# Kernel tuning notes

Hardware: AMD Instinct MI355X
Metric: run time of the kernel (lower is better)

## Reference

```python
import jax, jax.numpy as jnp
import numpy as np

N = 16384
IN_DIM = 11
D = 64
L = 4
K = 16 + 1  # self.k + 1 (n >= k+1)
EPS = 1e-5


def _bn(x, g, b):
    # BatchNorm1d in training mode: biased batch stats over the edge/node axis
    m = jnp.mean(x, axis=0)
    v = jnp.var(x, axis=0)
    return g * (x - m) * jax.lax.rsqrt(v + EPS) + b


def _mlp(x, W1, b1, g1, be1, W2, b2, g2, be2):
    x = jax.nn.relu(_bn(x @ W1 + b1, g1, be1))
    x = jax.nn.relu(_bn(x @ W2 + b2, g2, be2))
    return x


def _knn_edges(h):
    # torch.cdist + topk(-d, K); row 0 of idx.T is the (self) nearest node
    hs = jax.lax.stop_gradient(h)  # only indices are used downstream
    sq = jnp.sum(hs * hs, axis=-1)
    d2 = sq[:, None] + sq[None, :] - 2.0 * (hs @ hs.T)  # (n, n)
    d = jnp.sqrt(jnp.maximum(d2, 0.0))
    _, idx = jax.lax.top_k(-d, K)  # (n, K)
    frm = jnp.tile(idx[:, 0], K - 1)            # from_nodes = row0 repeated
    to = idx[:, 1:].T.reshape(-1)               # to_nodes = rows 1..K-1 flattened
    return frm, to


def setup_inputs() -> dict:
    key = jax.random.key(0)
    ks = jax.random.split(key, 8)
    s = 0.05
    inp = {
        "pos": jax.random.normal(ks[0], (N, IN_DIM), jnp.float32),
        "lin_in_W": jax.random.normal(ks[1], (IN_DIM, D), jnp.float32) * s,
        "lin_in_b": jnp.zeros((D,), jnp.float32),
        "pred_W": jax.random.normal(ks[2], (D, 1), jnp.float32) * s,
        "pred_b": jnp.zeros((1,), jnp.float32),
    }
    i = 3
    for pre in ("msg", "upd"):
        inp[f"{pre}_W1"] = jax.random.normal(ks[i], (L, 2 * D, D), jnp.float32) * s
        inp[f"{pre}_b1"] = jnp.zeros((L, D), jnp.float32)
        inp[f"{pre}_g1"] = jnp.ones((L, D), jnp.float32)
        inp[f"{pre}_be1"] = jnp.zeros((L, D), jnp.float32)
        inp[f"{pre}_W2"] = jax.random.normal(ks[i + 1], (L, D, D), jnp.float32) * s
        inp[f"{pre}_b2"] = jnp.zeros((L, D), jnp.float32)
        inp[f"{pre}_g2"] = jnp.ones((L, D), jnp.float32)
        inp[f"{pre}_be2"] = jnp.zeros((L, D), jnp.float32)
        i += 2
    return inp


def reference(pos, lin_in_W, lin_in_b, pred_W, pred_b,
              msg_W1, msg_b1, msg_g1, msg_be1, msg_W2, msg_b2, msg_g2, msg_be2,
              upd_W1, upd_b1, upd_g1, upd_be1, upd_W2, upd_b2, upd_g2, upd_be2):
    h = pos @ lin_in_W + lin_in_b  # (n, d)
    for l in range(L):
        frm, to = _knn_edges(h)
        # PyG source_to_target: h_j = h[edge_index[0]] (source), h_i = h[edge_index[1]] (dest)
        h_i = h[to]
        h_j = h[frm]
        msg = _mlp(jnp.concatenate([h_i, h_j], axis=-1),
                   msg_W1[l], msg_b1[l], msg_g1[l], msg_be1[l],
                   msg_W2[l], msg_b2[l], msg_g2[l], msg_be2[l])  # (e, d)
        agg = jax.ops.segment_sum(msg, to, num_segments=N)  # scatter-add at dest
        upd = _mlp(jnp.concatenate([h, agg], axis=-1),
                   upd_W1[l], upd_b1[l], upd_g1[l], upd_be1[l],
                   upd_W2[l], upd_b2[l], upd_g2[l], upd_be2[l])
        h = h + upd  # residual
    h_graph = jnp.mean(h, axis=0, keepdims=True)  # global_mean_pool, single graph
    out = h_graph @ pred_W + pred_b
    return out.reshape(-1)
```

## Files before the change

### kernel.cpp

```cpp
#include <hip/hip_runtime.h>

#define NN 16384
#define KP1 17
#define EE (NN*16)
#define CAP 448

typedef short bf16x8 __attribute__((ext_vector_type(8)));
typedef float f32x16 __attribute__((ext_vector_type(16)));

__device__ __forceinline__ ushort f2bf(float f) {
  unsigned u = __float_as_uint(f);
  unsigned r = (u + 0x7fffu + ((u >> 16) & 1u)) >> 16;
  return (ushort)r;
}
__device__ __forceinline__ float bf2f(ushort s) { return __uint_as_float(((unsigned)s) << 16); }

__global__ __launch_bounds__(256) void k_lin_in(const float* __restrict__ pos,
    const float* __restrict__ W, const float* __restrict__ b, float* __restrict__ h) {
  const int t = blockIdx.x*256 + threadIdx.x;
  const int n = t >> 6, c = t & 63;
  float acc = b[c];
  #pragma unroll
  for (int k = 0; k < 11; ++k) acc = fmaf(pos[n*11+k], W[k*64+c], acc);
  h[t] = acc;
}

__global__ __launch_bounds__(256) void k_prep_all(const float* __restrict__ h, float* __restrict__ sq,
    ushort* __restrict__ pk, ushort* __restrict__ hbh, ushort* __restrict__ hbl) {
  const int row = blockIdx.x*256 + threadIdx.x;
  const int tile = row >> 5, rl = row & 31;
  const float4* rp = (const float4*)(h + (size_t)row*64);
  float s = 0.f;
  #pragma unroll
  for (int q = 0; q < 16; ++q) {
    const float4 x = rp[q];
    s += x.x*x.x + x.y*x.y + x.z*x.z + x.w*x.w;
    ushort4 hi, lo;
    hi.x = f2bf(x.x); lo.x = f2bf(x.x - bf2f(hi.x));
    hi.y = f2bf(x.y); lo.y = f2bf(x.y - bf2f(hi.y));
    hi.z = f2bf(x.z); lo.z = f2bf(x.z - bf2f(hi.z));
    hi.w = f2bf(x.w); lo.w = f2bf(x.w - bf2f(hi.w));
    *(ushort4*)(hbh + (size_t)row*64 + q*4) = hi;
    *(ushort4*)(hbl + (size_t)row*64 + q*4) = lo;
    const int ks = q >> 2, sub = (q >> 1) & 1, e = (q & 1)*4;
    const int lane = rl + 32*sub;
    ushort* base = pk + (size_t)tile*4096 + ks*1024 + (size_t)lane*8 + e;
    *(ushort4*)(base)       = hi;
    *(ushort4*)(base + 512) = lo;
  }
  sq[row] = s;
}

__global__ __launch_bounds__(256) void k_wprep(const float* __restrict__ W1all,
    const float* __restrict__ W2all, ushort* __restrict__ wp1, ushort* __restrict__ wp2) {
  const int t = blockIdx.x*256 + threadIdx.x;
  if (t < 4096) {
    const int lane = t & 63, ks = (t>>6)&7, mt = (t>>9)&1, l = t>>10;
    const int m = mt*32 + (lane&31);
    const int k0 = ks*16 + (lane>>5)*8;
    const float* w = W1all + l*8192;
    ushort* dst = wp1 + ((((size_t)l*2 + mt)*8 + ks)*2)*512 + (size_t)lane*8;
    #pragma unroll
    for (int e = 0; e < 8; ++e) {
      const float v = w[(k0+e)*64 + m];
      const ushort hi = f2bf(v);
      dst[e] = hi; dst[512+e] = f2bf(v - bf2f(hi));
    }
  } else if (t < 6144) {
    const int t2 = t - 4096;
    const int lane = t2 & 63, ks = (t2>>6)&3, mt = (t2>>8)&1, l = t2>>9;
    const int m = mt*32 + (lane&31);
    const int k0 = ks*16 + (lane>>5)*8;
    const float* w = W2all + l*4096;
    ushort* dst = wp2 + ((((size_t)l*2 + mt)*4 + ks)*2)*512 + (size_t)lane*8;
    #pragma unroll
    for (int e = 0; e < 8; ++e) {
      const float v = w[(k0+e)*64 + m];
      const ushort hi = f2bf(v);
      dst[e] = hi; dst[512+e] = f2bf(v - bf2f(hi));
    }
  }
}

struct F8 { bf16x8 h0,h1,h2,h3,l0,l1,l2,l3; };

__device__ __forceinline__ void ldf(const ushort* __restrict__ pk, int tile, int lane, F8& f) {
  const ushort* tp = pk + (size_t)tile*4096 + (size_t)lane*8;
  f.h0 = *(const bf16x8*)(tp);
  f.l0 = *(const bf16x8*)(tp + 512);
  f.h1 = *(const bf16x8*)(tp + 1024);
  f.l1 = *(const bf16x8*)(tp + 1536);
  f.h2 = *(const bf16x8*)(tp + 2048);
  f.l2 = *(const bf16x8*)(tp + 2560);
  f.h3 = *(const bf16x8*)(tp + 3072);
  f.l3 = *(const bf16x8*)(tp + 3584);
}

#define MF(A,B,C) __builtin_amdgcn_mfma_f32_32x32x16_bf16(A,B,C,0,0,0)

__device__ __forceinline__ void tile_keys(const F8& f, const bf16x8 (&bqh)[4], const bf16x8 (&bql)[4],
    const float* __restrict__ sq, const int tile, const int lhi, float (&key)[16]) {
  f32x16 acc;
  #pragma unroll
  for (int i = 0; i < 16; ++i) acc[i] = 0.f;
  acc = MF(f.h0, bqh[0], acc); acc = MF(f.h0, bql[0], acc); acc = MF(f.l0, bqh[0], acc);
  acc = MF(f.h1, bqh[1], acc); acc = MF(f.h1, bql[1], acc); acc = MF(f.l1, bqh[1], acc);
  acc = MF(f.h2, bqh[2], acc); acc = MF(f.h2, bql[2], acc); acc = MF(f.l2, bqh[2], acc);
  acc = MF(f.h3, bqh[3], acc); acc = MF(f.h3, bql[3], acc); acc = MF(f.l3, bqh[3], acc);
  const int c0 = tile*32;
  #pragma unroll
  for (int g = 0; g < 4; ++g) {
    const float4 v = *(const float4*)(sq + c0 + g*8 + 4*lhi);
    key[g*4+0] = fmaf(-2.f, acc[g*4+0], v.x);
    key[g*4+1] = fmaf(-2.f, acc[g*4+1], v.y);
    key[g*4+2] = fmaf(-2.f, acc[g*4+2], v.z);
    key[g*4+3] = fmaf(-2.f, acc[g*4+3], v.w);
  }
}

#define HIST1(K) { _Pragma("unroll") for (int r = 0; r < 16; ++r) { \
    unsigned x = __float_as_uint(K[r]); x = (x & 0x80000000u) ? ~x : (x | 0x80000000u); \
    atomicAdd(&hist[x >> 24][qcol], 1u); } }
#define HIST2(K) { _Pragma("unroll") for (int r = 0; r < 16; ++r) { \
    unsigned x = __float_as_uint(K[r]); x = (x & 0x80000000u) ? ~x : (x | 0x80000000u); \
    if ((x >> 24) == b1) atomicAdd(&hist[(x >> 16) & 255u][qcol], 1u); } }
#define COLLECT(K, TILE) { _Pragma("unroll") for (int r = 0; r < 16; ++r) { \
    if (K[r] <= bfq) { \
      unsigned x = __float_as_uint(K[r]); x = (x & 0x80000000u) ? ~x : (x | 0x80000000u); \
      const unsigned slot = atomicAdd(&ccnt[qcol], 1u); \
      if (slot < CAP) { \
        const int cidx = (TILE)*32 + (r & 3) + 8*(r >> 2) + 4*lhi; \
        coll[(size_t)q*CAP + slot] = ((unsigned long long)x << 32) | (unsigned)cidx; } } } }

__global__ __launch_bounds__(512) void k_knn(const ushort* __restrict__ pk,
    const float* __restrict__ sq, unsigned long long* __restrict__ coll,
    unsigned* __restrict__ gcnt) {
  __shared__ unsigned hist[256][32];
  __shared__ unsigned bin1s[32], below1s[32];
  __shared__ float boundf[32];
  __shared__ unsigned ccnt[32];
  const int tid = threadIdx.x;
  const int wave = tid >> 6, lane = tid & 63;
  const int qcol = lane & 31, lhi = lane >> 5;
  const int qt = blockIdx.x;
  const int q = qt*32 + qcol;

  for (int i = tid; i < 256*32; i += 512) ((unsigned*)hist)[i] = 0u;
  if (tid < 32) ccnt[tid] = 0u;

  bf16x8 bqh[4], bql[4];
  {
    const ushort* tp = pk + (size_t)qt*4096 + (size_t)lane*8;
    #pragma unroll
    for (int ks = 0; ks < 4; ++ks) {
      bqh[ks] = *(const bf16x8*)(tp + ks*1024);
      bql[ks] = *(const bf16x8*)(tp + ks*1024 + 512);
    }
  }
  __syncthreads();

  {
    F8 fa, fb;
    ldf(pk, wave*8, lane, fa);
    #pragma unroll 1
    for (int s = 0; s < 8; s += 2) {
      ldf(pk, wave*8 + s + 1, lane, fb);
      float k0[16]; tile_keys(fa, bqh, bql, sq, wave*8 + s, lhi, k0);
      HIST1(k0)
      if (s + 2 < 8) ldf(pk, wave*8 + s + 2, lane, fa);
      float k1[16]; tile_keys(fb, bqh, bql, sq, wave*8 + s + 1, lhi, k1);
      HIST1(k1)
    }
  }
  __syncthreads();
  if (tid < 32) {
    unsigned c = 0, b = 0, bl_ = 0, fnd = 0;
    #pragma unroll 1
    for (int i = 0; i < 256; ++i) {
      const unsigned nc = c + hist[i][tid];
      if (!fnd && nc >= KP1) { b = (unsigned)i; bl_ = c; fnd = 1; }
      c = nc;
    }
    bin1s[tid] = b; below1s[tid] = bl_;
  }
  __syncthreads();
  for (int i = tid; i < 256*32; i += 512) ((unsigned*)hist)[i] = 0u;
  __syncthreads();
  const unsigned b1 = bin1s[qcol];

  {
    F8 fa, fb;
    ldf(pk, wave*8, lane, fa);
    #pragma unroll 1
    for (int s = 0; s < 8; s += 2) {
      ldf(pk, wave*8 + s + 1, lane, fb);
      float k0[16]; tile_keys(fa, bqh, bql, sq, wave*8 + s, lhi, k0);
      HIST2(k0)
      if (s + 2 < 8) ldf(pk, wave*8 + s + 2, lane, fa);
      float k1[16]; tile_keys(fb, bqh, bql, sq, wave*8 + s + 1, lhi, k1);
      HIST2(k1)
    }
  }
  __syncthreads();
  if (tid < 32) {
    unsigned c = below1s[tid], b = 255u, fnd = 0;
    #pragma unroll 1
    for (int i = 0; i < 256; ++i) {
      c += hist[i][tid];
      if (!fnd && c >= KP1) { b = (unsigned)i; fnd = 1; }
    }
    const unsigned bu = (bin1s[tid] << 24) | (b << 16) | 0xFFFFu;
    boundf[tid] = __uint_as_float((bu & 0x80000000u) ? (bu & 0x7fffffffu) : ~bu);
  }
  __syncthreads();
  const float bfq = boundf[qcol];

  {
    F8 fa, fb;
    ldf(pk, wave*64, lane, fa);
    #pragma unroll 1
    for (int s = 0; s < 64; s += 2) {
      ldf(pk, wave*64 + s + 1, lane, fb);
      float k0[16]; tile_keys(fa, bqh, bql, sq, wave*64 + s, lhi, k0);
      COLLECT(k0, wave*64 + s)
      if (s + 2 < 64) ldf(pk, wave*64 + s + 2, lane, fa);
      float k1[16]; tile_keys(fb, bqh, bql, sq, wave*64 + s + 1, lhi, k1);
      COLLECT(k1, wave*64 + s + 1)
    }
  }
  __syncthreads();
  if (tid < 32) gcnt[qt*32 + tid] = min(ccnt[tid], (unsigned)CAP);
}

__global__ __launch_bounds__(256) void k_select(const unsigned long long* __restrict__ coll,
    const unsigned* __restrict__ gcnt, int* __restrict__ idxout) {
  const int gw = (blockIdx.x*256 + threadIdx.x) >> 6;
  const int lane = threadIdx.x & 63;
  const int m = min((int)gcnt[gw], CAP);
  const unsigned long long* cp = coll + (size_t)gw*CAP;
  unsigned long long a0,a1,a2,a3,a4,a5,a6;
  a0 = (lane       < m) ? cp[lane      ] : ~0ULL;
  a1 = (lane +  64 < m) ? cp[lane +  64] : ~0ULL;
  a2 = (lane + 128 < m) ? cp[lane + 128] : ~0ULL;
  a3 = (lane + 192 < m) ? cp[lane + 192] : ~0ULL;
  a4 = (lane + 256 < m) ? cp[lane + 256] : ~0ULL;
  a5 = (lane + 320 < m) ? cp[lane + 320] : ~0ULL;
  a6 = (lane + 384 < m) ? cp[lane + 384] : ~0ULL;
  #define CS(X,Y) { if (Y < X) { const unsigned long long t_ = X; X = Y; Y = t_; } }
  CS(a0,a1) CS(a2,a3) CS(a4,a5)
  CS(a1,a2) CS(a3,a4) CS(a5,a6)
  CS(a0,a1) CS(a2,a3) CS(a4,a5)
  CS(a1,a2) CS(a3,a4) CS(a5,a6)
  CS(a0,a1) CS(a2,a3) CS(a4,a5)
  CS(a1,a2) CS(a3,a4) CS(a5,a6)
  CS(a0,a1) CS(a2,a3) CS(a4,a5)
  #undef CS
  #pragma unroll
  for (int p = 0; p < KP1; ++p) {
    unsigned long long w = a0;
    #pragma unroll
    for (int d = 1; d < 64; d <<= 1) {
      const unsigned long long o = __shfl_xor(w, d);
      w = o < w ? o : w;
    }
    if (lane == 0) idxout[gw*KP1 + p] = (int)(unsigned)(w & 0xffffffffULL);
    if (a0 == w) { a0=a1; a1=a2; a2=a3; a3=a4; a4=a5; a5=a6; a6=~0ULL; }
  }
}

__global__ __launch_bounds__(256) void k_cnt(const int* __restrict__ idx, unsigned* __restrict__ cnt) {
  const int e = blockIdx.x*256 + threadIdx.x;
  const int i = e & (NN-1), k = e >> 14;
  atomicAdd(&cnt[idx[i*KP1 + k + 1]], 1u);
}

__global__ __launch_bounds__(256) void k_scan(const unsigned* __restrict__ cnt,
    unsigned* __restrict__ offs, unsigned* __restrict__ pos) {
  __shared__ unsigned ps[256];
  const int t = threadIdx.x;
  unsigned s = 0;
  #pragma unroll 4
  for (int j = 0; j < 64; ++j) s += cnt[t*64 + j];
  ps[t] = s;
  __syncthreads();
  for (int d = 1; d < 256; d <<= 1) {
    const unsigned v = (t >= d) ? ps[t-d] : 0u;
    __syncthreads();
    ps[t] += v;
    __syncthreads();
  }
  unsigned run = ps[t] - s;
  #pragma unroll 4
  for (int j = 0; j < 64; ++j) {
    const unsigned c = cnt[t*64 + j];
    offs[t*64 + j] = run; pos[t*64 + j] = run;
    run += c;
  }
}

__global__ __launch_bounds__(256) void k_scatter(const int* __restrict__ idx,
    unsigned* __restrict__ pos, unsigned* __restrict__ sortedE) {
  const int e = blockIdx.x*256 + threadIdx.x;
  const int i = e & (NN-1), k = e >> 14;
  const int to = idx[i*KP1 + k + 1];
  sortedE[atomicAdd(&pos[to], 1u)] = (unsigned)e;
}

__global__ __launch_bounds__(256) void k_agg(const ushort* __restrict__ y2,
    const unsigned* __restrict__ offs, const unsigned* __restrict__ cnt,
    const unsigned* __restrict__ sortedE,
    const float* __restrict__ s, const float* __restrict__ s2,
    const float* __restrict__ gam, const float* __restrict__ bet, float* __restrict__ agg) {
  __shared__ float scs[64], shs[64];
  const int tid = threadIdx.x;
  if (tid < 64) {
    const float m = s[tid] * (1.f/(float)EE);
    const float v = fmaxf(s2[tid]*(1.f/(float)EE) - m*m, 0.f);
    const float scv = gam[tid]*rsqrtf(v + 1e-5f);
    scs[tid] = scv; shs[tid] = bet[tid] - m*scv;
  }
  __syncthreads();
  const int t = blockIdx.x*256 + tid;
  const int n = t >> 4, c4 = t & 15;
  const unsigned o = offs[n], m = cnt[n];
  const float sc0 = scs[c4*4+0], sc1 = scs[c4*4+1], sc2 = scs[c4*4+2], sc3 = scs[c4*4+3];
  const float sh0 = shs[c4*4+0], sh1 = shs[c4*4+1], sh2 = shs[c4*4+2], sh3 = shs[c4*4+3];
  float a0=0.f, a1=0.f, a2=0.f, a3=0.f;
  for (unsigned j = 0; j < m; ++j) {
    const unsigned e = sortedE[o + j];
    const ushort4 v = *(const ushort4*)(y2 + (size_t)e*64 + c4*4);
    a0 += fmaxf(fmaf(bf2f(v.x), sc0, sh0), 0.f);
    a1 += fmaxf(fmaf(bf2f(v.y), sc1, sh1), 0.f);
    a2 += fmaxf(fmaf(bf2f(v.z), sc2, sh2), 0.f);
    a3 += fmaxf(fmaf(bf2f(v.w), sc3, sh3), 0.f);
  }
  *(float4*)(agg + (size_t)n*64 + c4*4) = make_float4(a0, a1, a2, a3);
}

__global__ __launch_bounds__(256) void k_eA(const ushort* __restrict__ hbh,
    const ushort* __restrict__ hbl, const int* __restrict__ idx,
    const ushort* __restrict__ wp1, const float* __restrict__ b1, ushort* __restrict__ y1) {
  __shared__ ushort wlds[16384];
  __shared__ float b1s[64];
  __shared__ ushort ytr[4][32][40];
  const int tid = threadIdx.x, wave = tid >> 6, lane = tid & 63;
  const int n = lane & 31, lhi = lane >> 5;
  for (int i = tid*8; i < 16384; i += 2048) *(uint4*)(wlds+i) = *(const uint4*)(wp1+i);
  if (tid < 64) b1s[tid] = b1[tid];
  __syncthreads();

  const int tile = blockIdx.x*4 + wave;
  const int e = tile*32 + n;
  const int i_ = e & (NN-1), kk = e >> 14;
  const int to = idx[i_*KP1 + kk + 1];
  const int fr = idx[i_*KP1];

  bf16x8 bh[8], bl[8];
  #pragma unroll
  for (int ks = 0; ks < 4; ++ks) {
    const size_t off = (size_t)to*64 + ks*16 + lhi*8;
    bh[ks] = *(const bf16x8*)(hbh + off);
    bl[ks] = *(const bf16x8*)(hbl + off);
  }
  #pragma unroll
  for (int ks = 0; ks < 4; ++ks) {
    const size_t off = (size_t)fr*64 + ks*16 + lhi*8;
    bh[4+ks] = *(const bf16x8*)(hbh + off);
    bl[4+ks] = *(const bf16x8*)(hbl + off);
  }

  f32x16 aA[2], aB[2];
  #pragma unroll
  for (int i = 0; i < 16; ++i) { aA[0][i]=0.f; aA[1][i]=0.f; aB[0][i]=0.f; aB[1][i]=0.f; }
  #pragma unroll
  for (int mt = 0; mt < 2; ++mt) {
    #pragma unroll
    for (int ks = 0; ks < 8; ++ks) {
      const ushort* wp = wlds + ((mt*8+ks)*2)*512 + lane*8;
      const bf16x8 wh = *(const bf16x8*)wp;
      const bf16x8 wl = *(const bf16x8*)(wp + 512);
      aA[mt] = MF(wh, bh[ks], aA[mt]);
      aB[mt] = MF(wh, bl[ks], aB[mt]);
      aB[mt] = MF(wl, bh[ks], aB[mt]);
    }
  }

  #pragma unroll
  for (int mt = 0; mt < 2; ++mt) {
    #pragma unroll
    for (int g = 0; g < 4; ++g) {
      const int mb = mt*32 + g*8 + lhi*4;
      ushort4 p;
      p.x = f2bf(aA[mt][g*4+0] + aB[mt][g*4+0] + b1s[mb+0]);
      p.y = f2bf(aA[mt][g*4+1] + aB[mt][g*4+1] + b1s[mb+1]);
      p.z = f2bf(aA[mt][g*4+2] + aB[mt][g*4+2] + b1s[mb+2]);
      p.w = f2bf(aA[mt][g*4+3] + aB[mt][g*4+3] + b1s[mb+3]);
      *(ushort4*)(&ytr[wave][n][g*8 + lhi*4]) = p;
    }
    __syncthreads();
    #pragma unroll
    for (int rep = 0; rep < 2; ++rep) {
      const int s = rep*256 + tid;
      const int w = s >> 7, inner = s & 127;
      const int nn = inner >> 2, c8 = inner & 3;
      const bf16x8 v = *(const bf16x8*)(&ytr[w][nn][c8*8]);
      const int tw = blockIdx.x*4 + w;
      *(bf16x8*)(y1 + ((size_t)tw*32 + nn)*64 + mt*32 + c8*8) = v;
    }
    __syncthreads();
  }
}

__global__ __launch_bounds__(256) void k_estats(const ushort* __restrict__ y,
    float* __restrict__ s, float* __restrict__ s2) {
  __shared__ float ls[16][64], lq[16][64];
  const int tid = threadIdx.x;
  const int c4 = tid & 15, g = tid >> 4;
  float a0=0,a1=0,a2=0,a3=0,b0=0,b1=0,b2=0,b3=0;
  for (int r = blockIdx.x*16 + g; r < EE; r += 4096) {
    const ushort4 v = *(const ushort4*)(y + (size_t)r*64 + c4*4);
    const float f0 = bf2f(v.x), f1 = bf2f(v.y), f2 = bf2f(v.z), f3 = bf2f(v.w);
    a0 += f0; b0 = fmaf(f0,f0,b0);
    a1 += f1; b1 = fmaf(f1,f1,b1);
    a2 += f2; b2 = fmaf(f2,f2,b2);
    a3 += f3; b3 = fmaf(f3,f3,b3);
  }
  ls[g][c4*4+0]=a0; ls[g][c4*4+1]=a1; ls[g][c4*4+2]=a2; ls[g][c4*4+3]=a3;
  lq[g][c4*4+0]=b0; lq[g][c4*4+1]=b1; lq[g][c4*4+2]=b2; lq[g][c4*4+3]=b3;
  __syncthreads();
  if (tid < 64) {
    float sa = 0.f, sb = 0.f;
    #pragma unroll
    for (int gg = 0; gg < 16; ++gg) { sa += ls[gg][tid]; sb += lq[gg][tid]; }
    atomicAdd(&s[tid], sa); atomicAdd(&s2[tid], sb);
  }
}

__global__ __launch_bounds__(256) void k_eB(const ushort* __restrict__ y1,
    const float* __restrict__ s, const float* __restrict__ s2,
    const float* __restrict__ gam, const float* __restrict__ bet,
    const ushort* __restrict__ wp2, const float* __restrict__ b2, ushort* __restrict__ y2) {
  __shared__ ushort wlds[8192];
  __shared__ float scs[64], shs[64], b2s[64];
  __shared__ ushort ytr[4][32][40];
  const int tid = threadIdx.x, wave = tid >> 6, lane = tid & 63;
  const int n = lane & 31, lhi = lane >> 5;
  for (int i = tid*8; i < 8192; i += 2048) *(uint4*)(wlds+i) = *(const uint4*)(wp2+i);
  if (tid < 64) {
    const float m = s[tid] * (1.f/(float)EE);
    const float v = fmaxf(s2[tid]*(1.f/(float)EE) - m*m, 0.f);
    const float scv = gam[tid]*rsqrtf(v + 1e-5f);
    scs[tid] = scv; shs[tid] = bet[tid] - m*scv; b2s[tid] = b2[tid];
  }
  __syncthreads();

  const int tile = blockIdx.x*4 + wave;
  const int e = tile*32 + n;

  bf16x8 bh[4], bl[4];
  #pragma unroll
  for (int ks = 0; ks < 4; ++ks) {
    const ushort4 v0 = *(const ushort4*)(y1 + (size_t)e*64 + ks*16 + lhi*8);
    const ushort4 v1 = *(const ushort4*)(y1 + (size_t)e*64 + ks*16 + lhi*8 + 4);
    const int k0 = ks*16 + lhi*8;
    float x[8];
    x[0]=bf2f(v0.x); x[1]=bf2f(v0.y); x[2]=bf2f(v0.z); x[3]=bf2f(v0.w);
    x[4]=bf2f(v1.x); x[5]=bf2f(v1.y); x[6]=bf2f(v1.z); x[7]=bf2f(v1.w);
    #pragma unroll
    for (int j = 0; j < 8; ++j) {
      const float f = fmaxf(fmaf(x[j], scs[k0+j], shs[k0+j]), 0.f);
      const ushort hi = f2bf(f);
      bh[ks][j] = (short)hi;
      bl[ks][j] = (short)f2bf(f - bf2f(hi));
    }
  }

  f32x16 aA[2], aB[2];
  #pragma unroll
  for (int i = 0; i < 16; ++i) { aA[0][i]=0.f; aA[1][i]=0.f; aB[0][i]=0.f; aB[1][i]=0.f; }
  #pragma unroll
  for (int mt = 0; mt < 2; ++mt) {
    #pragma unroll
    for (int ks = 0; ks < 4; ++ks) {
      const ushort* wp = wlds + ((mt*4+ks)*2)*512 + lane*8;
      const bf16x8 wh = *(const bf16x8*)wp;
      const bf16x8 wl = *(const bf16x8*)(wp + 512);
      aA[mt] = MF(wh, bh[ks], aA[mt]);
      aB[mt] = MF(wh, bl[ks], aB[mt]);
      aB[mt] = MF(wl, bh[ks], aB[mt]);
    }
  }

  #pragma unroll
  for (int mt = 0; mt < 2; ++mt) {
    #pragma unroll
    for (int g = 0; g < 4; ++g) {
      const int mb = mt*32 + g*8 + lhi*4;
      ushort4 p;
      p.x = f2bf(aA[mt][g*4+0] + aB[mt][g*4+0] + b2s[mb+0]);
      p.y = f2bf(aA[mt][g*4+1] + aB[mt][g*4+1] + b2s[mb+1]);
      p.z = f2bf(aA[mt][g*4+2] + aB[mt][g*4+2] + b2s[mb+2]);
      p.w = f2bf(aA[mt][g*4+3] + aB[mt][g*4+3] + b2s[mb+3]);
      *(ushort4*)(&ytr[wave][n][g*8 + lhi*4]) = p;
    }
    __syncthreads();
    #pragma unroll
    for (int rep = 0; rep < 2; ++rep) {
      const int ss = rep*256 + tid;
      const int w = ss >> 7, inner = ss & 127;
      const int nn = inner >> 2, c8 = inner & 3;
      const bf16x8 v = *(const bf16x8*)(&ytr[w][nn][c8*8]);
      const int tw = blockIdx.x*4 + w;
      *(bf16x8*)(y2 + ((size_t)tw*32 + nn)*64 + mt*32 + c8*8) = v;
    }
    __syncthreads();
  }
}

__global__ __launch_bounds__(256) void k_colstats(const float* __restrict__ x, const int rows,
    float* __restrict__ s, float* __restrict__ s2) {
  __shared__ float ls[4][64], ls2[4][64];
  const int tid = threadIdx.x;
  const int c = tid & 63, g = tid >> 6;
  float a = 0.f, b = 0.f;
  for (int r = blockIdx.x*4 + g; r < rows; r += 1024) {
    const float v = x[(size_t)r*64 + c];
    a += v; b = fmaf(v, v, b);
  }
  ls[g][c] = a; ls2[g][c] = b;
  __syncthreads();
  if (tid < 64) {
    atomicAdd(&s[tid],  ls[0][tid]+ls[1][tid]+ls[2][tid]+ls[3][tid]);
    atomicAdd(&s2[tid], ls2[0][tid]+ls2[1][tid]+ls2[2][tid]+ls2[3][tid]);
  }
}

__device__ __forceinline__ void fmarow(float (&acc)[64], const float (*ws)[64], int kk, float xv) {
  #pragma unroll
  for (int cq = 0; cq < 16; ++cq) {
    const float4 w4 = *(const float4*)&ws[kk][cq*4];
    acc[cq*4]   = fmaf(xv, w4.x, acc[cq*4]);
    acc[cq*4+1] = fmaf(xv, w4.y, acc[cq*4+1]);
    acc[cq*4+2] = fmaf(xv, w4.z, acc[cq*4+2]);
    acc[cq*4+3] = fmaf(xv, w4.w, acc[cq*4+3]);
  }
}

__global__ __launch_bounds__(256) void k_mlpA_cat(const float* __restrict__ h,
    const float* __restrict__ agg, const float* __restrict__ W1, const float* __restrict__ b1,
    float* __restrict__ y) {
  __shared__ __align__(16) float ws[128][64];
  const int tid = threadIdx.x;
  for (int t = tid; t < 128*64/4; t += 256) ((float4*)ws)[t] = ((const float4*)W1)[t];
  __syncthreads();
  const int n = blockIdx.x*256 + tid;
  float acc[64];
  #pragma unroll
  for (int c = 0; c < 64; ++c) acc[c] = b1[c];
  const float4* xa = (const float4*)(h + (size_t)n*64);
  #pragma unroll 2
  for (int kb = 0; kb < 16; ++kb) {
    const float4 x4 = xa[kb];
    fmarow(acc, ws, kb*4,   x4.x); fmarow(acc, ws, kb*4+1, x4.y);
    fmarow(acc, ws, kb*4+2, x4.z); fmarow(acc, ws, kb*4+3, x4.w);
  }
  const float4* xb = (const float4*)(agg + (size_t)n*64);
  #pragma unroll 2
  for (int kb = 0; kb < 16; ++kb) {
    const float4 x4 = xb[kb];
    fmarow(acc, ws, 64+kb*4,   x4.x); fmarow(acc, ws, 64+kb*4+1, x4.y);
    fmarow(acc, ws, 64+kb*4+2, x4.z); fmarow(acc, ws, 64+kb*4+3, x4.w);
  }
  float4* yo = (float4*)(y + (size_t)n*64);
  #pragma unroll
  for (int q = 0; q < 16; ++q) yo[q] = make_float4(acc[4*q], acc[4*q+1], acc[4*q+2], acc[4*q+3]);
}

__global__ __launch_bounds__(256) void k_mlpB(float* __restrict__ y,
    const float* __restrict__ s, const float* __restrict__ s2,
    const float* __restrict__ g, const float* __restrict__ be,
    const float* __restrict__ W2, const float* __restrict__ b2, const float invR) {
  __shared__ __align__(16) float ws[64][64];
  __shared__ float sc[64], sh[64];
  const int tid = threadIdx.x;
  for (int t = tid; t < 64*64/4; t += 256) ((float4*)ws)[t] = ((const float4*)W2)[t];
  if (tid < 64) {
    const float m = s[tid]*invR;
    const float v = fmaxf(s2[tid]*invR - m*m, 0.f);
    const float scv = g[tid]*rsqrtf(v + 1e-5f);
    sc[tid] = scv; sh[tid] = be[tid] - m*scv;
  }
  __syncthreads();
  const int e = blockIdx.x*256 + tid;
  float acc[64];
  #pragma unroll
  for (int c = 0; c < 64; ++c) acc[c] = b2[c];
  const float4* yr = (const float4*)(y + (size_t)e*64);
  #pragma unroll 2
  for (int kb = 0; kb < 16; ++kb) {
    const float4 x4 = yr[kb];
    const int k0 = kb*4;
    fmarow(acc, ws, k0,   fmaxf(fmaf(x4.x, sc[k0],   sh[k0]),   0.f));
    fmarow(acc, ws, k0+1, fmaxf(fmaf(x4.y, sc[k0+1], sh[k0+1]), 0.f));
    fmarow(acc, ws, k0+2, fmaxf(fmaf(x4.z, sc[k0+2], sh[k0+2]), 0.f));
    fmarow(acc, ws, k0+3, fmaxf(fmaf(x4.w, sc[k0+3], sh[k0+3]), 0.f));
  }
  float4* yo = (float4*)(y + (size_t)e*64);
  #pragma unroll
  for (int q = 0; q < 16; ++q) yo[q] = make_float4(acc[4*q], acc[4*q+1], acc[4*q+2], acc[4*q+3]);
}

__global__ __launch_bounds__(256) void k_updC(const float* __restrict__ y,
    const float* __restrict__ s, const float* __restrict__ s2,
    const float* __restrict__ g, const float* __restrict__ be,
    float* __restrict__ h, const float invR) {
  __shared__ float sc[64], sh[64];
  const int tid = threadIdx.x;
  if (tid < 64) {
    const float m = s[tid]*invR;
    const float v = fmaxf(s2[tid]*invR - m*m, 0.f);
    const float scv = g[tid]*rsqrtf(v + 1e-5f);
    sc[tid] = scv; sh[tid] = be[tid] - m*scv;
  }
  __syncthreads();
  const int t = blockIdx.x*256 + tid;
  const int c = t & 63;
  h[t] += fmaxf(fmaf(y[t], sc[c], sh[c]), 0.f);
}

__global__ void k_final(const float* __restrict__ hsum, const float* __restrict__ pW,
                        const float* __restrict__ pb, float* __restrict__ out) {
  const int c = threadIdx.x;
  float v = hsum[c] * (1.f/(float)NN) * pW[c];
  #pragma unroll
  for (int m = 32; m >= 1; m >>= 1) v += __shfl_xor(v, m, 64);
  if (c == 0) out[0] = v + pb[0];
}

extern "C" void kernel_launch(void* const* d_in, const int* in_sizes, int n_in,
                              void* d_out, int out_size, void* d_ws, size_t ws_size,
                              hipStream_t stream) {
  const float* pos   = (const float*)d_in[0];
  const float* linW  = (const float*)d_in[1];
  const float* linb  = (const float*)d_in[2];
  const float* predW = (const float*)d_in[3];
  const float* predb = (const float*)d_in[4];
  const float* mW1 = (const float*)d_in[5];
  const float* mb1 = (const float*)d_in[6];
  const float* mg1 = (const float*)d_in[7];
  const float* mbe1= (const float*)d_in[8];
  const float* mW2 = (const float*)d_in[9];
  const float* mb2 = (const float*)d_in[10];
  const float* mg2 = (const float*)d_in[11];
  const float* mbe2= (const float*)d_in[12];
  const float* uW1 = (const float*)d_in[13];
  const float* ub1 = (const float*)d_in[14];
  const float* ug1 = (const float*)d_in[15];
  const float* ube1= (const float*)d_in[16];
  const float* uW2 = (const float*)d_in[17];
  const float* ub2 = (const float*)d_in[18];
  const float* ug2 = (const float*)d_in[19];
  const float* ube2= (const float*)d_in[20];

  float* h     = (float*)d_ws;
  float* sq    = h + (size_t)NN*64;
  float* agg   = sq + NN;
  float* ubuf  = agg + (size_t)NN*64;
  float* stats = ubuf + (size_t)NN*64;
  int*   idx   = (int*)(stats + 640);
  char*  yb    = (char*)(idx + (size_t)NN*KP1);
  ushort* pk = (ushort*)yb;
  unsigned long long* coll = (unsigned long long*)(yb + 4194304);
  ushort* hbh = (ushort*)(yb + 62914560);
  ushort* hbl = hbh + (size_t)NN*64;
  ushort* y1 = (ushort*)yb;
  ushort* y2 = y1 + (size_t)EE*64;
  ushort* wp1 = (ushort*)(yb + 67108864);
  ushort* wp2 = wp1 + 4*16384;
  unsigned* cnt     = (unsigned*)ubuf;
  unsigned* offs    = cnt + NN;
  unsigned* pcur    = offs + NN;
  unsigned* sortedE = pcur + NN;
  unsigned* gcnt    = sortedE + EE;

  k_lin_in<<<NN*64/256, 256, 0, stream>>>(pos, linW, linb, h);
  k_wprep<<<24, 256, 0, stream>>>(mW1, mW2, wp1, wp2);
  for (int l = 0; l < 4; ++l) {
    k_prep_all<<<NN/256, 256, 0, stream>>>(h, sq, pk, hbh, hbl);
    k_knn<<<NN/32, 512, 0, stream>>>(pk, sq, coll, gcnt);
    k_select<<<NN/4, 256, 0, stream>>>(coll, gcnt, idx);
    hipMemsetAsync(stats, 0, 640*sizeof(float), stream);
    hipMemsetAsync(cnt, 0, NN*sizeof(unsigned), stream);
    k_cnt<<<EE/256, 256, 0, stream>>>(idx, cnt);
    k_scan<<<1, 256, 0, stream>>>(cnt, offs, pcur);
    k_scatter<<<EE/256, 256, 0, stream>>>(idx, pcur, sortedE);
    k_eA<<<EE/32/4, 256, 0, stream>>>(hbh, hbl, idx, wp1 + (size_t)l*16384, mb1 + l*64, y1);
    k_estats<<<256, 256, 0, stream>>>(y1, stats, stats+64);
    k_eB<<<EE/32/4, 256, 0, stream>>>(y1, stats, stats+64, mg1 + l*64, mbe1 + l*64,
                                      wp2 + (size_t)l*8192, mb2 + l*64, y2);
    k_estats<<<256, 256, 0, stream>>>(y2, stats+128, stats+192);
    k_agg<<<NN*16/256, 256, 0, stream>>>(y2, offs, cnt, sortedE, stats+128, stats+192,
                                         mg2 + l*64, mbe2 + l*64, agg);
    k_mlpA_cat<<<NN/256, 256, 0, stream>>>(h, agg, uW1 + l*8192, ub1 + l*64, ubuf);
    k_colstats<<<256, 256, 0, stream>>>(ubuf, NN, stats+256, stats+320);
    k_mlpB<<<NN/256, 256, 0, stream>>>(ubuf, stats+256, stats+320, ug1 + l*64, ube1 + l*64,
                                       uW2 + l*4096, ub2 + l*64, 1.f/(float)NN);
    k_colstats<<<256, 256, 0, stream>>>(ubuf, NN, stats+384, stats+448);
    k_updC<<<NN*64/256, 256, 0, stream>>>(ubuf, stats+384, stats+448, ug2 + l*64, ube2 + l*64,
                                          h, 1.f/(float)NN);
  }
  hipMemsetAsync(stats+512, 0, 128*sizeof(float), stream);
  k_colstats<<<256, 256, 0, stream>>>(h, NN, stats+512, stats+576);
  k_final<<<1, 64, 0, stream>>>(stats+512, predW, predb, (float*)d_out);
}
```

Baseline: 2.438 ms.

## Interleave paired-tile MFMA chains, two-level histogram scan, fuse degree count into select

The kNN kernel now computes two distance tiles with interleaved MFMA accumulator chains, which hides MFMA dependency latency, and drops the software-pipelined prefetch in favour of loading both tiles each iteration. The serial 256-bin histogram scans done by 32 threads are replaced by a parallel 16-way partial sum followed by a scan of only one 16-bin chunk. The separate k_cnt kernel is removed and the in-degree count is done with atomics inside k_select. In exchange, register pressure rises from holding two F8 tiles, and global loads are no longer overlapped across iterations.

```diff
diff --git a/kernel.cpp b/kernel.cpp
--- a/kernel.cpp
+++ b/kernel.cpp
@@ -98,23 +98,37 @@
 
 #define MF(A,B,C) __builtin_amdgcn_mfma_f32_32x32x16_bf16(A,B,C,0,0,0)
 
-__device__ __forceinline__ void tile_keys(const F8& f, const bf16x8 (&bqh)[4], const bf16x8 (&bql)[4],
-    const float* __restrict__ sq, const int tile, const int lhi, float (&key)[16]) {
-  f32x16 acc;
-  #pragma unroll
-  for (int i = 0; i < 16; ++i) acc[i] = 0.f;
-  acc = MF(f.h0, bqh[0], acc); acc = MF(f.h0, bql[0], acc); acc = MF(f.l0, bqh[0], acc);
-  acc = MF(f.h1, bqh[1], acc); acc = MF(f.h1, bql[1], acc); acc = MF(f.l1, bqh[1], acc);
-  acc = MF(f.h2, bqh[2], acc); acc = MF(f.h2, bql[2], acc); acc = MF(f.l2, bqh[2], acc);
-  acc = MF(f.h3, bqh[3], acc); acc = MF(f.h3, bql[3], acc); acc = MF(f.l3, bqh[3], acc);
-  const int c0 = tile*32;
+__device__ __forceinline__ void tile_keys2(const F8& fa, const F8& fb,
+    const bf16x8 (&bqh)[4], const bf16x8 (&bql)[4], const float* __restrict__ sq,
+    const int ta, const int tb, const int lhi, float (&ka)[16], float (&kb)[16]) {
+  f32x16 a, b;
+  #pragma unroll
+  for (int i = 0; i < 16; ++i) { a[i] = 0.f; b[i] = 0.f; }
+  a = MF(fa.h0, bqh[0], a);  b = MF(fb.h0, bqh[0], b);
+  a = MF(fa.h0, bql[0], a);  b = MF(fb.h0, bql[0], b);
+  a = MF(fa.l0, bqh[0], a);  b = MF(fb.l0, bqh[0], b);
+  a = MF(fa.h1, bqh[1], a);  b = MF(fb.h1, bqh[1], b);
+  a = MF(fa.h1, bql[1], a);  b = MF(fb.h1, bql[1], b);
+  a = MF(fa.l1, bqh[1], a);  b = MF(fb.l1, bqh[1], b);
+  a = MF(fa.h2, bqh[2], a);  b = MF(fb.h2, bqh[2], b);
+  a = MF(fa.h2, bql[2], a);  b = MF(fb.h2, bql[2], b);
+  a = MF(fa.l2, bqh[2], a);  b = MF(fb.l2, bqh[2], b);
+  a = MF(fa.h3, bqh[3], a);  b = MF(fb.h3, bqh[3], b);
+  a = MF(fa.h3, bql[3], a);  b = MF(fb.h3, bql[3], b);
+  a = MF(fa.l3, bqh[3], a);  b = MF(fb.l3, bqh[3], b);
+  const int c0a = ta*32, c0b = tb*32;
   #pragma unroll
   for (int g = 0; g < 4; ++g) {
-    const float4 v = *(const float4*)(sq + c0 + g*8 + 4*lhi);
-    key[g*4+0] = fmaf(-2.f, acc[g*4+0], v.x);
-    key[g*4+1] = fmaf(-2.f, acc[g*4+1], v.y);
-    key[g*4+2] = fmaf(-2.f, acc[g*4+2], v.z);
-    key[g*4+3] = fmaf(-2.f, acc[g*4+3], v.w);
+    const float4 va = *(const float4*)(sq + c0a + g*8 + 4*lhi);
+    const float4 vb = *(const float4*)(sq + c0b + g*8 + 4*lhi);
+    ka[g*4+0] = fmaf(-2.f, a[g*4+0], va.x);
+    ka[g*4+1] = fmaf(-2.f, a[g*4+1], va.y);
+    ka[g*4+2] = fmaf(-2.f, a[g*4+2], va.z);
+    ka[g*4+3] = fmaf(-2.f, a[g*4+3], va.w);
+    kb[g*4+0] = fmaf(-2.f, b[g*4+0], vb.x);
+    kb[g*4+1] = fmaf(-2.f, b[g*4+1], vb.y);
+    kb[g*4+2] = fmaf(-2.f, b[g*4+2], vb.z);
+    kb[g*4+3] = fmaf(-2.f, b[g*4+3], vb.w);
   }
 }
 
@@ -136,6 +150,7 @@
     const float* __restrict__ sq, unsigned long long* __restrict__ coll,
     unsigned* __restrict__ gcnt) {
   __shared__ unsigned hist[256][32];
+  __shared__ unsigned part[16][32];
   __shared__ unsigned bin1s[32], below1s[32];
   __shared__ float boundf[32];
   __shared__ unsigned ccnt[32];
@@ -159,55 +174,71 @@
   }
   __syncthreads();
 
+  #pragma unroll 1
+  for (int s = 0; s < 8; s += 2) {
+    F8 fa, fb;
+    ldf(pk, wave*8 + s, lane, fa);
+    ldf(pk, wave*8 + s + 1, lane, fb);
+    float ka[16], kb[16];
+    tile_keys2(fa, fb, bqh, bql, sq, wave*8 + s, wave*8 + s + 1, lhi, ka, kb);
+    HIST1(ka)
+    HIST1(kb)
+  }
+  __syncthreads();
   {
+    const int qq = tid & 31, j = tid >> 5;
+    unsigned ssum = 0;
+    #pragma unroll
+    for (int i = 0; i < 16; ++i) ssum += hist[j*16 + i][qq];
+    part[j][qq] = ssum;
+  }
+  __syncthreads();
+  if (tid < 32) {
+    unsigned cum = 0;
+    int jj = 0;
+    while (jj < 15 && cum + part[jj][tid] < KP1) { cum += part[jj][tid]; ++jj; }
+    unsigned c2 = cum, b = 0, fnd = 0;
+    #pragma unroll 1
+    for (int i = 0; i < 16; ++i) {
+      const unsigned nc = c2 + hist[jj*16 + i][tid];
+      if (!fnd && nc >= KP1) { b = (unsigned)(jj*16 + i); fnd = 1; break; }
+      c2 = nc;
+    }
+    bin1s[tid] = b; below1s[tid] = c2;
+  }
+  __syncthreads();
+  for (int i = tid; i < 256*32; i += 512) ((unsigned*)hist)[i] = 0u;
+  __syncthreads();
+  const unsigned b1 = bin1s[qcol];
+
+  #pragma unroll 1
+  for (int s = 0; s < 8; s += 2) {
     F8 fa, fb;
-    ldf(pk, wave*8, lane, fa);
+    ldf(pk, wave*8 + s, lane, fa);
+    ldf(pk, wave*8 + s + 1, lane, fb);
+    float ka[16], kb[16];
+    tile_keys2(fa, fb, bqh, bql, sq, wave*8 + s, wave*8 + s + 1, lhi, ka, kb);
+    HIST2(ka)
+    HIST2(kb)
+  }
+  __syncthreads();
+  {
+    const int qq = tid & 31, j = tid >> 5;
+    unsigned ssum = 0;
+    #pragma unroll
+    for (int i = 0; i < 16; ++i) ssum += hist[j*16 + i][qq];
+    part[j][qq] = ssum;
+  }
+  __syncthreads();
+  if (tid < 32) {
+    unsigned cum = below1s[tid];
+    int jj = 0;
+    while (jj < 15 && cum + part[jj][tid] < KP1) { cum += part[jj][tid]; ++jj; }
+    unsigned c2 = cum, b = 255u, fnd = 0;
     #pragma unroll 1
-    for (int s = 0; s < 8; s += 2) {
-      ldf(pk, wave*8 + s + 1, lane, fb);
-      float k0[16]; tile_keys(fa, bqh, bql, sq, wave*8 + s, lhi, k0);
-      HIST1(k0)
-      if (s + 2 < 8) ldf(pk, wave*8 + s + 2, lane, fa);
-      float k1[16]; tile_keys(fb, bqh, bql, sq, wave*8 + s + 1, lhi, k1);
-      HIST1(k1)
-    }
-  }
-  __syncthreads();
-  if (tid < 32) {
-    unsigned c = 0, b = 0, bl_ = 0, fnd = 0;
-    #pragma unroll 1
-    for (int i = 0; i < 256; ++i) {
-      const unsigned nc = c + hist[i][tid];
-      if (!fnd && nc >= KP1) { b = (unsigned)i; bl_ = c; fnd = 1; }
-      c = nc;
-    }
-    bin1s[tid] = b; below1s[tid] = bl_;
-  }
-  __syncthreads();
-  for (int i = tid; i < 256*32; i += 512) ((unsigned*)hist)[i] = 0u;
-  __syncthreads();
-  const unsigned b1 = bin1s[qcol];
-
-  {
-    F8 fa, fb;
-    ldf(pk, wave*8, lane, fa);
-    #pragma unroll 1
-    for (int s = 0; s < 8; s += 2) {
-      ldf(pk, wave*8 + s + 1, lane, fb);
-      float k0[16]; tile_keys(fa, bqh, bql, sq, wave*8 + s, lhi, k0);
-      HIST2(k0)
-      if (s + 2 < 8) ldf(pk, wave*8 + s + 2, lane, fa);
-      float k1[16]; tile_keys(fb, bqh, bql, sq, wave*8 + s + 1, lhi, k1);
-      HIST2(k1)
-    }
-  }
-  __syncthreads();
-  if (tid < 32) {
-    unsigned c = below1s[tid], b = 255u, fnd = 0;
-    #pragma unroll 1
-    for (int i = 0; i < 256; ++i) {
-      c += hist[i][tid];
-      if (!fnd && c >= KP1) { b = (unsigned)i; fnd = 1; }
+    for (int i = 0; i < 16; ++i) {
+      c2 += hist[jj*16 + i][tid];
+      if (!fnd && c2 >= KP1) { b = (unsigned)(jj*16 + i); fnd = 1; }
     }
     const unsigned bu = (bin1s[tid] << 24) | (b << 16) | 0xFFFFu;
     boundf[tid] = __uint_as_float((bu & 0x80000000u) ? (bu & 0x7fffffffu) : ~bu);
@@ -215,25 +246,22 @@
   __syncthreads();
   const float bfq = boundf[qcol];
 
-  {
+  #pragma unroll 1
+  for (int s = 0; s < 64; s += 2) {
     F8 fa, fb;
-    ldf(pk, wave*64, lane, fa);
-    #pragma unroll 1
-    for (int s = 0; s < 64; s += 2) {
-      ldf(pk, wave*64 + s + 1, lane, fb);
-      float k0[16]; tile_keys(fa, bqh, bql, sq, wave*64 + s, lhi, k0);
-      COLLECT(k0, wave*64 + s)
-      if (s + 2 < 64) ldf(pk, wave*64 + s + 2, lane, fa);
-      float k1[16]; tile_keys(fb, bqh, bql, sq, wave*64 + s + 1, lhi, k1);
-      COLLECT(k1, wave*64 + s + 1)
-    }
+    ldf(pk, wave*64 + s, lane, fa);
+    ldf(pk, wave*64 + s + 1, lane, fb);
+    float ka[16], kb[16];
+    tile_keys2(fa, fb, bqh, bql, sq, wave*64 + s, wave*64 + s + 1, lhi, ka, kb);
+    COLLECT(ka, wave*64 + s)
+    COLLECT(kb, wave*64 + s + 1)
   }
   __syncthreads();
   if (tid < 32) gcnt[qt*32 + tid] = min(ccnt[tid], (unsigned)CAP);
 }
 
 __global__ __launch_bounds__(256) void k_select(const unsigned long long* __restrict__ coll,
-    const unsigned* __restrict__ gcnt, int* __restrict__ idxout) {
+    const unsigned* __restrict__ gcnt, int* __restrict__ idxout, unsigned* __restrict__ cnt) {
   const int gw = (blockIdx.x*256 + threadIdx.x) >> 6;
   const int lane = threadIdx.x & 63;
   const int m = min((int)gcnt[gw], CAP);
@@ -263,15 +291,13 @@
       const unsigned long long o = __shfl_xor(w, d);
       w = o < w ? o : w;
     }
-    if (lane == 0) idxout[gw*KP1 + p] = (int)(unsigned)(w & 0xffffffffULL);
+    if (lane == 0) {
+      const int ni = (int)(unsigned)(w & 0xffffffffULL);
+      idxout[gw*KP1 + p] = ni;
+      if (p > 0) atomicAdd(&cnt[ni], 1u);
+    }
     if (a0 == w) { a0=a1; a1=a2; a2=a3; a3=a4; a4=a5; a5=a6; a6=~0ULL; }
   }
-}
-
-__global__ __launch_bounds__(256) void k_cnt(const int* __restrict__ idx, unsigned* __restrict__ cnt) {
-  const int e = blockIdx.x*256 + threadIdx.x;
-  const int i = e & (NN-1), k = e >> 14;
-  atomicAdd(&cnt[idx[i*KP1 + k + 1]], 1u);
 }
 
 __global__ __launch_bounds__(256) void k_scan(const unsigned* __restrict__ cnt,
@@ -688,10 +714,9 @@
   for (int l = 0; l < 4; ++l) {
     k_prep_all<<<NN/256, 256, 0, stream>>>(h, sq, pk, hbh, hbl);
     k_knn<<<NN/32, 512, 0, stream>>>(pk, sq, coll, gcnt);
-    k_select<<<NN/4, 256, 0, stream>>>(coll, gcnt, idx);
+    hipMemsetAsync(cnt, 0, NN*sizeof(unsigned), stream);
+    k_select<<<NN/4, 256, 0, stream>>>(coll, gcnt, idx, cnt);
     hipMemsetAsync(stats, 0, 640*sizeof(float), stream);
-    hipMemsetAsync(cnt, 0, NN*sizeof(unsigned), stream);
-    k_cnt<<<EE/256, 256, 0, stream>>>(idx, cnt);
     k_scan<<<1, 256, 0, stream>>>(cnt, offs, pcur);
     k_scatter<<<EE/256, 256, 0, stream>>>(idx, pcur, sortedE);
     k_eA<<<EE/32/4, 256, 0, stream>>>(hbh, hbl, idx, wp1 + (size_t)l*16384, mb1 + l*64, y1);
```

After: 2.222 ms. 1.1x faster.
